# Optimization experiments

Hardware: AMD Instinct MI355X
Metric: run time of the kernel (lower is better)

The kernel has to match this reference:

```python
import jax, jax.numpy as jnp
import numpy as np

R_MAX = 5.0
NUM_BASIS = 8
CUTOFF_P = 6
N_LAYERS = 3
C = 64          # hidden_mul / channels of irreps_conv_out (64x0e+64x1o)
Z = 4           # element_number
AVG_DEG = 32.0  # num-neighbor normalization (E/N)
SQRT3 = 1.7320508075688772
SQRT2 = 1.4142135623730951


def _radial_embedding(r):
    # Bessel basis * polynomial cutoff (RadialEdgeEmbedding)
    rs = jnp.maximum(r, 1e-9)
    n = jnp.arange(1, NUM_BASIS + 1, dtype=r.dtype)  # (B,)
    bessel = jnp.sqrt(2.0 / R_MAX) * jnp.sin(n * jnp.pi * rs[:, None] / R_MAX) / rs[:, None]
    x = r / R_MAX
    p = float(CUTOFF_P)
    fc = (1.0
          - (p + 1.0) * (p + 2.0) / 2.0 * x ** CUTOFF_P
          + p * (p + 2.0) * x ** (CUTOFF_P + 1)
          - p * (p + 1.0) / 2.0 * x ** (CUTOFF_P + 2))
    fc = jnp.where(x < 1.0, fc, 0.0)
    return bessel * fc[:, None]  # (E, NUM_BASIS)


def setup_inputs() -> dict:
    key = jax.random.key(0)
    ks = jax.random.split(key, 20)
    N, E, B = 16000, 512000, 16
    atom_type = jax.random.randint(ks[0], (N,), 0, Z)
    # atoms in a 4A box so most edge lengths fall inside r_max=5
    atom_pos = jax.random.uniform(ks[1], (N, 3), dtype=jnp.float32) * 4.0
    edge_src = jax.random.randint(ks[2], (E,), 0, N)
    edge_dst = jax.random.randint(ks[3], (E,), 0, N)
    edge_cell_shift = jnp.zeros((E, 3), jnp.float32)
    cell = jnp.tile(jnp.eye(3, dtype=jnp.float32) * 10.0, (B, 1, 1)) \
        + 0.01 * jax.random.normal(ks[4], (B, 3, 3), jnp.float32)
    image_index = jax.random.randint(ks[5], (N,), 0, B)
    g = lambda k, s, fan: jax.random.normal(k, s, jnp.float32) / np.sqrt(fan)
    return {
        'atom_type': atom_type, 'atom_pos': atom_pos,
        'edge_src': edge_src, 'edge_dst': edge_dst,
        'edge_cell_shift': edge_cell_shift, 'cell': cell, 'image_index': image_index,
        'w_lin_in': g(ks[6], (Z, C), Z),
        'mlp_w1': g(ks[7], (N_LAYERS, NUM_BASIS, 64), NUM_BASIS),
        'mlp_b1': jnp.zeros((N_LAYERS, 64), jnp.float32),
        'mlp_w2': g(ks[8], (N_LAYERS, 64, 5 * C), 64),
        'w_self_s': g(ks[9], (N_LAYERS, C, C), C),
        'w_self_v': g(ks[10], (N_LAYERS, C, C), C),
        'w_gate': g(ks[11], (N_LAYERS, C, C), C),
        'w_lin1': g(ks[12], (C, 16), C),
        'w_lin2': g(ks[13], (16, 1), 16),
    }


def reference(atom_type, atom_pos, edge_src, edge_dst, edge_cell_shift, cell,
              image_index, w_lin_in, mlp_w1, mlp_b1, mlp_w2,
              w_self_s, w_self_v, w_gate, w_lin1, w_lin2):
    N = atom_pos.shape[0]
    # edge vectors with periodic cell shift
    edge_vec = atom_pos[edge_dst] - atom_pos[edge_src]
    edge_vec = edge_vec + jnp.einsum('ni,nij->nj', edge_cell_shift,
                                     cell.reshape(-1, 3, 3)[image_index[edge_src]])
    r = jnp.linalg.norm(edge_vec, axis=1)                      # (E,)
    unit = edge_vec / jnp.maximum(r, 1e-9)[:, None]
    # spherical harmonics lmax=1, component normalization: y0=1 (implicit), y1=sqrt(3)*unit
    y1 = SQRT3 * unit                                           # (E, 3)
    emb = _radial_embedding(r)                                  # (E, NUM_BASIS)

    # one-hot embedding + input linear (one-hot is all 0e -> scalar channels only)
    onehot = jax.nn.one_hot(atom_type, Z, dtype=atom_pos.dtype)
    s = onehot @ w_lin_in                                       # (N, C) l=0 features
    v = jnp.zeros((N, C, 3), atom_pos.dtype)                    # (N, C, 3) l=1 features

    inv_sqrt_deg = 1.0 / np.sqrt(AVG_DEG)
    for L in range(N_LAYERS):
        # radial MLP -> per-edge per-channel tensor-product path weights
        w = jax.nn.silu(emb @ mlp_w1[L] + mlp_b1[L]) @ mlp_w2[L]  # (E, 5C)
        w1, w2, w3, w4, w5 = jnp.split(w, 5, axis=1)              # (E, C) each
        s_src = s[edge_src]                                       # (E, C)
        v_src = v[edge_src]                                       # (E, C, 3)
        vdoty = jnp.einsum('ecx,ex->ec', v_src, y1)
        # CG tensor-product paths (l<=1):
        m_s = w1 * s_src + w2 * vdoty / SQRT3                     # 0x0->0, 1x1->0
        m_v = (w3[:, :, None] * s_src[:, :, None] * y1[:, None, :]      # 0x1->1
               + w4[:, :, None] * v_src                                  # 1x0->1
               + w5[:, :, None] * jnp.cross(v_src, y1[:, None, :]) / SQRT2)  # 1x1->1
        agg_s = jax.ops.segment_sum(m_s, edge_dst, num_segments=N) * inv_sqrt_deg
        agg_v = jax.ops.segment_sum(m_v, edge_dst, num_segments=N) * inv_sqrt_deg
        # gated self-interaction + resnet
        gate = jax.nn.sigmoid(agg_s @ w_gate[L])                  # (N, C)
        s = s + jax.nn.silu(agg_s @ w_self_s[L])
        v = v + jnp.einsum('ncx,cd->ndx', agg_v, w_self_v[L]) * gate[:, :, None]

    # o3.Linear to 16x0e then 1x0e (only scalar channels map to 0e outputs)
    atomic_energy = (s @ w_lin1) @ w_lin2                         # (N, 1)
    atomic_energy = atomic_energy * 1.0                           # atomic_scale
    return atomic_energy
```

## Files before the change

kernel.cpp:

```cpp
#include <hip/hip_runtime.h>
#include <hip/hip_fp16.h>
#include <math.h>

#define NUM_BASIS 8
#define SQRT3 1.7320508075688772f
#define SQRT2 1.4142135623730951f
#define INV_SQRT_DEG 0.17677669529663687f
#define PI_F 3.14159265358979323846f

typedef _Float16 half8 __attribute__((ext_vector_type(8)));
typedef float float4v __attribute__((ext_vector_type(4)));

__device__ __forceinline__ float sigmoidf_(float x) { return 1.0f / (1.0f + __expf(-x)); }
__device__ __forceinline__ float siluf_(float x) { return x * sigmoidf_(x); }

__device__ __forceinline__ void unp2(unsigned u, float& a, float& b) {
    __half2 h = *reinterpret_cast<__half2*>(&u);
    float2 f = __half22float2(h);
    a = f.x; b = f.y;
}
__device__ __forceinline__ unsigned pk2(float a, float b) {
    __half2 h = __floats2half2_rn(a, b);
    return *reinterpret_cast<unsigned*>(&h);
}

__global__ __launch_bounds__(256) void count_deg(
    const int* __restrict__ dst, int* __restrict__ deg, int E)
{
    int e = blockIdx.x * blockDim.x + threadIdx.x;
    if (e < E) atomicAdd(&deg[dst[e]], 1);
}

__global__ __launch_bounds__(1024) void scan_deg(
    const int* __restrict__ deg, int* __restrict__ cursor, int N)
{
    __shared__ int wsum[16];
    __shared__ int carry_s, tot_s;
    int tid = threadIdx.x;
    int wid = tid >> 6, lane = tid & 63;
    if (tid == 0) carry_s = 0;
    __syncthreads();
    for (int base = 0; base < N; base += 16384) {
        int i0 = base + tid * 16;
        int v[16];
        int sum = 0;
        #pragma unroll
        for (int k = 0; k < 16; k++) {
            int i = i0 + k;
            v[k] = (i < N) ? deg[i] : 0;
            sum += v[k];
        }
        int incl = sum;
        #pragma unroll
        for (int off = 1; off < 64; off <<= 1) {
            int t = __shfl_up(incl, off);
            if (lane >= off) incl += t;
        }
        if (lane == 63) wsum[wid] = incl;
        __syncthreads();
        if (wid == 0 && lane < 16) {
            int wv = wsum[lane];
            int wincl = wv;
            #pragma unroll
            for (int off = 1; off < 16; off <<= 1) {
                int t = __shfl_up(wincl, off);
                if (lane >= off) wincl += t;
            }
            wsum[lane] = wincl - wv;
            if (lane == 15) tot_s = wincl;
        }
        __syncthreads();
        int carry = carry_s;
        int run = carry + wsum[wid] + incl - sum;
        #pragma unroll
        for (int k = 0; k < 16; k++) {
            int i = i0 + k;
            if (i < N) cursor[i] = run;
            run += v[k];
        }
        __syncthreads();
        if (tid == 0) carry_s = carry + tot_s;
        __syncthreads();
    }
}

__global__ __launch_bounds__(256) void edge_pre_scatter(
    const float* __restrict__ pos, const int* __restrict__ src,
    const int* __restrict__ dst, const float* __restrict__ cs,
    const float* __restrict__ cell, const int* __restrict__ img,
    int* __restrict__ cursor, float* __restrict__ emb,
    float4* __restrict__ y14, int2* __restrict__ sdp, int E)
{
    int e = blockIdx.x * blockDim.x + threadIdx.x;
    if (e >= E) return;
    int si = src[e], di = dst[e];
    int slot = atomicAdd(&cursor[di], 1);
    sdp[slot] = make_int2(si, di);
    float vx = pos[di*3+0] - pos[si*3+0];
    float vy = pos[di*3+1] - pos[si*3+1];
    float vz = pos[di*3+2] - pos[si*3+2];
    float c0 = cs[(size_t)e*3+0], c1 = cs[(size_t)e*3+1], c2 = cs[(size_t)e*3+2];
    const float* M = cell + (size_t)img[si] * 9;
    vx += c0*M[0] + c1*M[3] + c2*M[6];
    vy += c0*M[1] + c1*M[4] + c2*M[7];
    vz += c0*M[2] + c1*M[5] + c2*M[8];
    float r  = sqrtf(vx*vx + vy*vy + vz*vz);
    float rs = fmaxf(r, 1e-9f);
    float inv = 1.0f / rs;
    y14[slot] = make_float4(SQRT3*vx*inv, SQRT3*vy*inv, SQRT3*vz*inv, 0.0f);
    float x = r * (1.0f / 5.0f);
    float x2 = x*x, x6 = x2*x2*x2;
    float fc = 1.0f - 28.0f*x6 + 48.0f*x6*x - 21.0f*x6*x2;
    if (x >= 1.0f) fc = 0.0f;
    float pre = sqrtf(2.0f / 5.0f) * inv * fc;
    float t = PI_F * rs * (1.0f / 5.0f);
    #pragma unroll
    for (int n = 1; n <= NUM_BASIS; n++)
        emb[(size_t)slot*NUM_BASIS + (n-1)] = pre * __sinf((float)n * t);
}

__global__ __launch_bounds__(256) void prep_weights(
    const float* __restrict__ W2, _Float16* __restrict__ w2f,
    const float* __restrict__ Wg, const float* __restrict__ Ws,
    const float* __restrict__ Wv, _Float16* __restrict__ wgtf,
    const float* __restrict__ Wl1, const float* __restrict__ Wl2,
    float* __restrict__ wl12)
{
    int idx = blockIdx.x * blockDim.x + threadIdx.x;
    if (idx < 64) {
        float a = 0.f;
        #pragma unroll
        for (int j = 0; j < 16; j++) a = fmaf(Wl1[idx*16 + j], Wl2[j], a);
        wl12[idx] = a;
    }
    if (idx < 3 * 20480) {
        int L  = idx / 20480;
        int r  = idx % 20480;
        int cg = r / 5120;
        int r2 = r % 5120;
        int p  = r2 / 1024;
        int r3 = r2 % 1024;
        int kh = r3 / 512;
        int r4 = r3 % 512;
        int lane = r4 / 8;
        int j  = r4 % 8;
        int k = kh*32 + (lane >> 4)*8 + j;
        int n = p*64 + cg*16 + (lane & 15);
        w2f[idx] = (_Float16)W2[(size_t)L*20480 + k*320 + n];
    } else if (idx < 3*20480 + 3*3*4096) {
        int idx2 = idx - 3*20480;
        int L   = idx2 / 12288;
        int rem = idx2 % 12288;
        int mat = rem / 4096;
        int r2  = rem % 4096;
        int cg  = r2 / 1024;
        int r3  = r2 % 1024;
        int kh  = r3 / 512;
        int r4  = r3 % 512;
        int lane = r4 / 8;
        int j   = r4 % 8;
        int k = kh*32 + (lane >> 4)*8 + j;
        int n = cg*16 + (lane & 15);
        const float* src = (mat == 0) ? Wg : (mat == 1) ? Ws : Wv;
        wgtf[idx2] = (_Float16)src[(size_t)L*4096 + k*64 + n];
    }
}

__device__ __forceinline__ void mlp1_afrag(
    const float* __restrict__ emb, const float* __restrict__ W1,
    const float* __restrict__ B1, int eA, int q, half8 afrag[2])
{
    float4 ea = *(const float4*)(emb + (size_t)eA*8);
    float4 eb2 = *(const float4*)(emb + (size_t)eA*8 + 4);
    float em[8] = {ea.x, ea.y, ea.z, ea.w, eb2.x, eb2.y, eb2.z, eb2.w};
    #pragma unroll
    for (int kh = 0; kh < 2; kh++) {
        int kb = kh*32 + q*8;
        float hv[8];
        float4 b0 = *(const float4*)(B1 + kb);
        float4 b1 = *(const float4*)(B1 + kb + 4);
        hv[0]=b0.x; hv[1]=b0.y; hv[2]=b0.z; hv[3]=b0.w;
        hv[4]=b1.x; hv[5]=b1.y; hv[6]=b1.z; hv[7]=b1.w;
        #pragma unroll
        for (int jj = 0; jj < 8; jj++) {
            float4 wa = *(const float4*)(W1 + jj*64 + kb);
            float4 wb = *(const float4*)(W1 + jj*64 + kb + 4);
            hv[0] = fmaf(em[jj], wa.x, hv[0]);
            hv[1] = fmaf(em[jj], wa.y, hv[1]);
            hv[2] = fmaf(em[jj], wa.z, hv[2]);
            hv[3] = fmaf(em[jj], wa.w, hv[3]);
            hv[4] = fmaf(em[jj], wb.x, hv[4]);
            hv[5] = fmaf(em[jj], wb.y, hv[5]);
            hv[6] = fmaf(em[jj], wb.z, hv[6]);
            hv[7] = fmaf(em[jj], wb.w, hv[7]);
        }
        #pragma unroll
        for (int j = 0; j < 8; j++)
            afrag[kh][j] = (_Float16)siluf_(hv[j]);
    }
}

__global__ __launch_bounds__(256) void edge_msg_mfma_l0(
    const float* __restrict__ emb, const float4* __restrict__ y14,
    const int2* __restrict__ sdp,
    const int* __restrict__ type, const float* __restrict__ wlin,
    const float* __restrict__ W1, const float* __restrict__ B1,
    const _Float16* __restrict__ w2f,
    float* __restrict__ aggs, float* __restrict__ aggx,
    float* __restrict__ aggy, float* __restrict__ aggz, int E)
{
    int wave  = (blockIdx.x * blockDim.x + threadIdx.x) >> 6;
    int lane  = threadIdx.x & 63;
    int wbase = wave * 16;
    if (wbase >= E) return;
    int q   = lane >> 4;
    int col = lane & 15;

    int eb = wbase + q*4;
    int d[4], tt[4];
    float4 y1v[4];
    #pragma unroll
    for (int r = 0; r < 4; r++) {
        int2 sv = sdp[eb + r];
        tt[r] = type[sv.x];
        d[r]  = sv.y;
        y1v[r] = y14[eb + r];
    }

    half8 afrag[2];
    mlp1_afrag(emb, W1, B1, wbase + col, q, afrag);

    int dnq = __shfl_down(d[0], 16);
    int nd3 = (q == 3) ? -1 : dnq;
    int df = d[0], dl = d[3];
    bool U = (df == dl);
    int dlp = __shfl_up(dl, 16);
    bool link = (q > 0) && (dlp == df);

    #pragma unroll
    for (int cg = 0; cg < 4; cg++) {
        float4v a1 = {0,0,0,0}, a3 = {0,0,0,0};
        const _Float16* wbp = w2f + ((size_t)cg*5*2*64*8) + (size_t)lane*8;
        {
            half8 b10 = *(const half8*)(wbp + ((size_t)(0*2 + 0))*64*8);
            half8 b11 = *(const half8*)(wbp + ((size_t)(0*2 + 1))*64*8);
            half8 b30 = *(const half8*)(wbp + ((size_t)(2*2 + 0))*64*8);
            half8 b31 = *(const half8*)(wbp + ((size_t)(2*2 + 1))*64*8);
            a1 = __builtin_amdgcn_mfma_f32_16x16x32_f16(afrag[0], b10, a1, 0, 0, 0);
            a1 = __builtin_amdgcn_mfma_f32_16x16x32_f16(afrag[1], b11, a1, 0, 0, 0);
            a3 = __builtin_amdgcn_mfma_f32_16x16x32_f16(afrag[0], b30, a3, 0, 0, 0);
            a3 = __builtin_amdgcn_mfma_f32_16x16x32_f16(afrag[1], b31, a3, 0, 0, 0);
        }
        int c = cg*16 + col;

        float ms[4], mx[4], my[4], mz[4];
        #pragma unroll
        for (int r = 0; r < 4; r++) {
            float s = wlin[tt[r]*64 + c];
            float w3s = a3[r] * s;
            ms[r] = a1[r] * s;
            mx[r] = w3s * y1v[r].x;
            my[r] = w3s * y1v[r].y;
            mz[r] = w3s * y1v[r].z;
        }
        #pragma unroll
        for (int r = 1; r < 4; r++) {
            if (d[r] == d[r-1]) {
                ms[r] += ms[r-1]; mx[r] += mx[r-1];
                my[r] += my[r-1]; mz[r] += mz[r-1];
            }
        }
        float Cs = 0.f, Cx = 0.f, Cy = 0.f, Cz = 0.f;
        #pragma unroll
        for (int it = 0; it < 3; it++) {
            float es = ms[3] + (U ? Cs : 0.f);
            float ex = mx[3] + (U ? Cx : 0.f);
            float ey = my[3] + (U ? Cy : 0.f);
            float ez = mz[3] + (U ? Cz : 0.f);
            float ts = __shfl_up(es, 16);
            float tx = __shfl_up(ex, 16);
            float ty = __shfl_up(ey, 16);
            float tz = __shfl_up(ez, 16);
            Cs = link ? ts : 0.f; Cx = link ? tx : 0.f;
            Cy = link ? ty : 0.f; Cz = link ? tz : 0.f;
        }
        bool hr = true;
        #pragma unroll
        for (int r = 0; r < 4; r++) {
            if (r > 0) hr = hr && (d[r] == d[r-1]);
            float fs = ms[r] + (hr ? Cs : 0.f);
            float fx = mx[r] + (hr ? Cx : 0.f);
            float fy = my[r] + (hr ? Cy : 0.f);
            float fz = mz[r] + (hr ? Cz : 0.f);
            int nd = (r < 3) ? d[r+1] : nd3;
            if (nd != d[r]) {
                size_t ai = (size_t)d[r]*64 + c;
                atomicAdd(aggs + ai, fs);
                atomicAdd(aggx + ai, fx);
                atomicAdd(aggy + ai, fy);
                atomicAdd(aggz + ai, fz);
            }
        }
    }
}

__global__ __launch_bounds__(256) void edge_msg_mfma(
    const float* __restrict__ emb, const float4* __restrict__ y14,
    const int2* __restrict__ sdp,
    const uint2* __restrict__ nf,
    const float* __restrict__ W1, const float* __restrict__ B1,
    const _Float16* __restrict__ w2f,
    float* __restrict__ aggs, float* __restrict__ aggx,
    float* __restrict__ aggy, float* __restrict__ aggz, int E)
{
    int wave  = (blockIdx.x * blockDim.x + threadIdx.x) >> 6;
    int lane  = threadIdx.x & 63;
    int wbase = wave * 16;
    if (wbase >= E) return;
    int q   = lane >> 4;
    int col = lane & 15;

    int eb = wbase + q*4;
    int d[4], si[4];
    float4 y1v[4];
    #pragma unroll
    for (int r = 0; r < 4; r++) {
        int2 sv = sdp[eb + r];
        si[r] = sv.x;
        d[r]  = sv.y;
        y1v[r] = y14[eb + r];
    }

    uint2 pf[4][4];
    #pragma unroll
    for (int r = 0; r < 4; r++) {
        size_t nb = (size_t)si[r] * 64 + col;
        pf[r][0] = nf[nb];
        pf[r][1] = nf[nb + 16];
        pf[r][2] = nf[nb + 32];
        pf[r][3] = nf[nb + 48];
    }

    half8 afrag[2];
    mlp1_afrag(emb, W1, B1, wbase + col, q, afrag);

    int dnq = __shfl_down(d[0], 16);
    int nd3 = (q == 3) ? -1 : dnq;
    int df = d[0], dl = d[3];
    bool U = (df == dl);
    int dlp = __shfl_up(dl, 16);
    bool link = (q > 0) && (dlp == df);

    #pragma unroll
    for (int cg = 0; cg < 4; cg++) {
        float4v acc[5];
        #pragma unroll
        for (int p = 0; p < 5; p++) acc[p] = (float4v){0.f, 0.f, 0.f, 0.f};
        const _Float16* wbp = w2f + ((size_t)cg*5*2*64*8) + (size_t)lane*8;
        #pragma unroll
        for (int p = 0; p < 5; p++) {
            half8 bf0 = *(const half8*)(wbp + ((size_t)(p*2 + 0))*64*8);
            half8 bf1 = *(const half8*)(wbp + ((size_t)(p*2 + 1))*64*8);
            acc[p] = __builtin_amdgcn_mfma_f32_16x16x32_f16(afrag[0], bf0, acc[p], 0, 0, 0);
            acc[p] = __builtin_amdgcn_mfma_f32_16x16x32_f16(afrag[1], bf1, acc[p], 0, 0, 0);
        }
        int c = cg*16 + col;

        float ms[4], mx[4], my[4], mz[4];
        #pragma unroll
        for (int r = 0; r < 4; r++) {
            float fsx, fvx, fvy, fvz;
            unp2(pf[r][cg].x, fsx, fvx);
            unp2(pf[r][cg].y, fvy, fvz);
            float yx = y1v[r].x, yy = y1v[r].y, yz = y1v[r].z;
            float w1 = acc[0][r], w2 = acc[1][r], w3 = acc[2][r];
            float w4 = acc[3][r], w5 = acc[4][r];
            float vdoty = fvx*yx + fvy*yy + fvz*yz;
            ms[r] = w1*fsx + w2*vdoty*(1.0f/SQRT3);
            float cx = fvy*yz - fvz*yy;
            float cy = fvz*yx - fvx*yz;
            float cz = fvx*yy - fvy*yx;
            mx[r] = w3*fsx*yx + w4*fvx + w5*cx*(1.0f/SQRT2);
            my[r] = w3*fsx*yy + w4*fvy + w5*cy*(1.0f/SQRT2);
            mz[r] = w3*fsx*yz + w4*fvz + w5*cz*(1.0f/SQRT2);
        }
        #pragma unroll
        for (int r = 1; r < 4; r++) {
            if (d[r] == d[r-1]) {
                ms[r] += ms[r-1]; mx[r] += mx[r-1];
                my[r] += my[r-1]; mz[r] += mz[r-1];
            }
        }
        float Cs = 0.f, Cx = 0.f, Cy = 0.f, Cz = 0.f;
        #pragma unroll
        for (int it = 0; it < 3; it++) {
            float es = ms[3] + (U ? Cs : 0.f);
            float ex = mx[3] + (U ? Cx : 0.f);
            float ey = my[3] + (U ? Cy : 0.f);
            float ez = mz[3] + (U ? Cz : 0.f);
            float ts = __shfl_up(es, 16);
            float tx = __shfl_up(ex, 16);
            float ty = __shfl_up(ey, 16);
            float tz = __shfl_up(ez, 16);
            Cs = link ? ts : 0.f; Cx = link ? tx : 0.f;
            Cy = link ? ty : 0.f; Cz = link ? tz : 0.f;
        }
        bool hr = true;
        #pragma unroll
        for (int r = 0; r < 4; r++) {
            if (r > 0) hr = hr && (d[r] == d[r-1]);
            float fs = ms[r] + (hr ? Cs : 0.f);
            float fx = mx[r] + (hr ? Cx : 0.f);
            float fy = my[r] + (hr ? Cy : 0.f);
            float fz = mz[r] + (hr ? Cz : 0.f);
            int nd = (r < 3) ? d[r+1] : nd3;
            if (nd != d[r]) {
                size_t ai = (size_t)d[r]*64 + c;
                atomicAdd(aggs + ai, fs);
                atomicAdd(aggx + ai, fx);
                atomicAdd(aggy + ai, fy);
                atomicAdd(aggz + ai, fz);
            }
        }
    }
}

__global__ __launch_bounds__(256) void node_update_mfma(
    uint2* __restrict__ nf,
    float* __restrict__ aggs, float* __restrict__ aggx,
    float* __restrict__ aggy, float* __restrict__ aggz,
    const _Float16* __restrict__ wgtf,
    const int* __restrict__ type, const float* __restrict__ wlin,
    const float* __restrict__ wl12,
    float* __restrict__ out, int first, int do_out, int N)
{
    int wave  = (blockIdx.x * blockDim.x + threadIdx.x) >> 6;
    int lane  = threadIdx.x & 63;
    int wbase = wave * 16;
    if (wbase >= N) return;
    int q = lane >> 4, col = lane & 15;

    int nodeA = wbase + col;
    if (nodeA >= N) nodeA = N - 1;
    size_t nb = (size_t)nodeA * 64 + q * 8;
    half8 af0[2], af1[2], af2[2], af3[2];
    #pragma unroll
    for (int kh = 0; kh < 2; kh++) {
        const float* p0 = aggs + nb + kh*32;
        const float* p1 = aggx + nb + kh*32;
        const float* p2 = aggy + nb + kh*32;
        const float* p3 = aggz + nb + kh*32;
        float4 a0 = *(const float4*)p0, b0 = *(const float4*)(p0+4);
        float4 a1 = *(const float4*)p1, b1 = *(const float4*)(p1+4);
        float4 a2 = *(const float4*)p2, b2 = *(const float4*)(p2+4);
        float4 a3 = *(const float4*)p3, b3 = *(const float4*)(p3+4);
        af0[kh][0]=(_Float16)(a0.x*INV_SQRT_DEG); af0[kh][1]=(_Float16)(a0.y*INV_SQRT_DEG);
        af0[kh][2]=(_Float16)(a0.z*INV_SQRT_DEG); af0[kh][3]=(_Float16)(a0.w*INV_SQRT_DEG);
        af0[kh][4]=(_Float16)(b0.x*INV_SQRT_DEG); af0[kh][5]=(_Float16)(b0.y*INV_SQRT_DEG);
        af0[kh][6]=(_Float16)(b0.z*INV_SQRT_DEG); af0[kh][7]=(_Float16)(b0.w*INV_SQRT_DEG);
        af1[kh][0]=(_Float16)(a1.x*INV_SQRT_DEG); af1[kh][1]=(_Float16)(a1.y*INV_SQRT_DEG);
        af1[kh][2]=(_Float16)(a1.z*INV_SQRT_DEG); af1[kh][3]=(_Float16)(a1.w*INV_SQRT_DEG);
        af1[kh][4]=(_Float16)(b1.x*INV_SQRT_DEG); af1[kh][5]=(_Float16)(b1.y*INV_SQRT_DEG);
        af1[kh][6]=(_Float16)(b1.z*INV_SQRT_DEG); af1[kh][7]=(_Float16)(b1.w*INV_SQRT_DEG);
        af2[kh][0]=(_Float16)(a2.x*INV_SQRT_DEG); af2[kh][1]=(_Float16)(a2.y*INV_SQRT_DEG);
        af2[kh][2]=(_Float16)(a2.z*INV_SQRT_DEG); af2[kh][3]=(_Float16)(a2.w*INV_SQRT_DEG);
        af2[kh][4]=(_Float16)(b2.x*INV_SQRT_DEG); af2[kh][5]=(_Float16)(b2.y*INV_SQRT_DEG);
        af2[kh][6]=(_Float16)(b2.z*INV_SQRT_DEG); af2[kh][7]=(_Float16)(b2.w*INV_SQRT_DEG);
        af3[kh][0]=(_Float16)(a3.x*INV_SQRT_DEG); af3[kh][1]=(_Float16)(a3.y*INV_SQRT_DEG);
        af3[kh][2]=(_Float16)(a3.z*INV_SQRT_DEG); af3[kh][3]=(_Float16)(a3.w*INV_SQRT_DEG);
        af3[kh][4]=(_Float16)(b3.x*INV_SQRT_DEG); af3[kh][5]=(_Float16)(b3.y*INV_SQRT_DEG);
        af3[kh][6]=(_Float16)(b3.z*INV_SQRT_DEG); af3[kh][7]=(_Float16)(b3.w*INV_SQRT_DEG);
    }

    int tt[4];
    #pragma unroll
    for (int r = 0; r < 4; r++) {
        int nd = wbase + q*4 + r;
        tt[r] = type[nd < N ? nd : 0];
    }

    float epart[4] = {0.f, 0.f, 0.f, 0.f};

    #pragma unroll
    for (int cg = 0; cg < 4; cg++) {
        const _Float16* bp = wgtf + (size_t)lane * 8;
        half8 bg0 = *(const half8*)(bp + ((size_t)((0*4 + cg)*2 + 0))*512);
        half8 bg1 = *(const half8*)(bp + ((size_t)((0*4 + cg)*2 + 1))*512);
        half8 bs0 = *(const half8*)(bp + ((size_t)((1*4 + cg)*2 + 0))*512);
        half8 bs1 = *(const half8*)(bp + ((size_t)((1*4 + cg)*2 + 1))*512);
        half8 bv0 = *(const half8*)(bp + ((size_t)((2*4 + cg)*2 + 0))*512);
        half8 bv1 = *(const half8*)(bp + ((size_t)((2*4 + cg)*2 + 1))*512);
        float4v ag = {0,0,0,0}, as = {0,0,0,0};
        float4v ox = {0,0,0,0}, oy = {0,0,0,0}, oz = {0,0,0,0};
        ag = __builtin_amdgcn_mfma_f32_16x16x32_f16(af0[0], bg0, ag, 0, 0, 0);
        ag = __builtin_amdgcn_mfma_f32_16x16x32_f16(af0[1], bg1, ag, 0, 0, 0);
        as = __builtin_amdgcn_mfma_f32_16x16x32_f16(af0[0], bs0, as, 0, 0, 0);
        as = __builtin_amdgcn_mfma_f32_16x16x32_f16(af0[1], bs1, as, 0, 0, 0);
        ox = __builtin_amdgcn_mfma_f32_16x16x32_f16(af1[0], bv0, ox, 0, 0, 0);
        ox = __builtin_amdgcn_mfma_f32_16x16x32_f16(af1[1], bv1, ox, 0, 0, 0);
        oy = __builtin_amdgcn_mfma_f32_16x16x32_f16(af2[0], bv0, oy, 0, 0, 0);
        oy = __builtin_amdgcn_mfma_f32_16x16x32_f16(af2[1], bv1, oy, 0, 0, 0);
        oz = __builtin_amdgcn_mfma_f32_16x16x32_f16(af3[0], bv0, oz, 0, 0, 0);
        oz = __builtin_amdgcn_mfma_f32_16x16x32_f16(af3[1], bv1, oz, 0, 0, 0);

        int c = cg*16 + col;
        float wlc = wl12[c];
        #pragma unroll
        for (int r = 0; r < 4; r++) {
            int nd = wbase + q*4 + r;
            bool wr = nd < N;
            size_t ni = (size_t)nd*64 + c;
            float sx, vx, vy, vz;
            if (first) {
                sx = wlin[tt[r]*64 + c];
                vx = 0.f; vy = 0.f; vz = 0.f;
            } else {
                uint2 cur = nf[wr ? ni : 0];
                unp2(cur.x, sx, vx);
                unp2(cur.y, vy, vz);
            }
            float gate = sigmoidf_(ag[r]);
            sx += siluf_(as[r]);
            vx += ox[r] * gate;
            vy += oy[r] * gate;
            vz += oz[r] * gate;
            if (wr) {
                uint2 nv;
                nv.x = pk2(sx, vx);
                nv.y = pk2(vy, vz);
                nf[ni] = nv;
                aggs[ni] = 0.f;
                aggx[ni] = 0.f;
                aggy[ni] = 0.f;
                aggz[ni] = 0.f;
                epart[r] = fmaf(sx, wlc, epart[r]);
            }
        }
    }
    if (do_out) {
        #pragma unroll
        for (int r = 0; r < 4; r++) {
            float e = epart[r];
            e += __shfl_xor(e, 1);
            e += __shfl_xor(e, 2);
            e += __shfl_xor(e, 4);
            e += __shfl_xor(e, 8);
            int nd = wbase + q*4 + r;
            if (col == 0 && nd < N) out[nd] = e;
        }
    }
}

extern "C" void kernel_launch(void* const* d_in, const int* in_sizes, int n_in,
                              void* d_out, int out_size, void* d_ws, size_t ws_size,
                              hipStream_t stream)
{
    const int*   atom_type = (const int*)  d_in[0];
    const float* pos       = (const float*)d_in[1];
    const int*   src       = (const int*)  d_in[2];
    const int*   dst       = (const int*)  d_in[3];
    const float* cs        = (const float*)d_in[4];
    const float* cell      = (const float*)d_in[5];
    const int*   img       = (const int*)  d_in[6];
    const float* wlin_in   = (const float*)d_in[7];
    const float* mw1       = (const float*)d_in[8];
    const float* mb1       = (const float*)d_in[9];
    const float* mw2       = (const float*)d_in[10];
    const float* wss       = (const float*)d_in[11];
    const float* wsv       = (const float*)d_in[12];
    const float* wg        = (const float*)d_in[13];
    const float* wl1       = (const float*)d_in[14];
    const float* wl2       = (const float*)d_in[15];
    int N = in_sizes[0];
    int E = in_sizes[2];

    char* w = (char*)d_ws;
    float*  emb  = (float*)w;  w += (size_t)E * 8 * sizeof(float);
    float4* y14  = (float4*)w; w += (size_t)E * sizeof(float4);
    int2*   sdp  = (int2*)w;   w += (size_t)E * sizeof(int2);
    uint2*  nf   = (uint2*)w;  w += (size_t)N * 64 * sizeof(uint2);
    float*  agg  = (float*)w;  w += (size_t)N * 64 * 4 * sizeof(float);
    _Float16* w2f  = (_Float16*)w; w += (size_t)3 * 20480 * sizeof(_Float16);
    _Float16* wgtf = (_Float16*)w; w += (size_t)3 * 3 * 4096 * sizeof(_Float16);
    float*  wl12 = (float*)w;  w += 64 * sizeof(float);
    int*    deg  = (int*)w;    w += (size_t)N * sizeof(int);
    int*    curs = (int*)w;    w += (size_t)N * sizeof(int);

    size_t NC = (size_t)N * 64;
    float* aggs = agg;
    float* aggx = agg + NC;
    float* aggy = agg + 2*NC;
    float* aggz = agg + 3*NC;

    hipMemsetAsync(deg, 0, (size_t)N * sizeof(int), stream);
    hipMemsetAsync(agg, 0, NC * 4 * sizeof(float), stream);
    count_deg<<<(E + 255) / 256, 256, 0, stream>>>(dst, deg, E);
    scan_deg<<<1, 1024, 0, stream>>>(deg, curs, N);
    int prep_n = 3*20480 + 3*3*4096;
    prep_weights<<<(prep_n + 255) / 256, 256, 0, stream>>>(
        mw2, w2f, wg, wss, wsv, wgtf, wl1, wl2, wl12);
    edge_pre_scatter<<<(E + 255) / 256, 256, 0, stream>>>(
        pos, src, dst, cs, cell, img, curs, emb, y14, sdp, E);

    int eblocks = (E + 63) / 64;
    int nblocks = (N + 63) / 64;

    edge_msg_mfma_l0<<<eblocks, 256, 0, stream>>>(
        emb, y14, sdp, atom_type, wlin_in,
        mw1, mb1, w2f, aggs, aggx, aggy, aggz, E);
    node_update_mfma<<<nblocks, 256, 0, stream>>>(
        nf, aggs, aggx, aggy, aggz, wgtf, atom_type, wlin_in, wl12,
        (float*)d_out, 1, 0, N);

    for (int L = 1; L < 3; L++) {
        edge_msg_mfma<<<eblocks, 256, 0, stream>>>(
            emb, y14, sdp, nf,
            mw1 + L * 8 * 64, mb1 + L * 64, w2f + (size_t)L * 20480,
            aggs, aggx, aggy, aggz, E);
        node_update_mfma<<<nblocks, 256, 0, stream>>>(
            nf, aggs, aggx, aggy, aggz,
            wgtf + (size_t)L * 12288, atom_type, wlin_in, wl12,
            (float*)d_out, 0, (L == 2) ? 1 : 0, N);
    }
}
```

Measured before the change: 525.7 us.

## Store edge embeddings and unit vectors in fp16 and drop cross-quad shuffle reduction

Edge radial embeddings and spherical-harmonic vectors are now stored as packed fp16 instead of fp32, halving their footprint and the bandwidth spent reading them in each of the three layers. The cross-quad carry chain built from wave shuffles is removed, so each quad of four edges now issues its own atomics when a destination run crosses a quad boundary. This cuts shuffle and select work but can raise atomic traffic on high-degree destinations, and fp16 storage lowers the precision of the geometric inputs.

Result: slower. 1.254 ms (+138.6%).

```diff
diff --git a/kernel.cpp b/kernel.cpp
--- a/kernel.cpp
+++ b/kernel.cpp
@@ -88,8 +88,8 @@
     const float* __restrict__ pos, const int* __restrict__ src,
     const int* __restrict__ dst, const float* __restrict__ cs,
     const float* __restrict__ cell, const int* __restrict__ img,
-    int* __restrict__ cursor, float* __restrict__ emb,
-    float4* __restrict__ y14, int2* __restrict__ sdp, int E)
+    int* __restrict__ cursor, _Float16* __restrict__ emb,
+    uint2* __restrict__ y14, int2* __restrict__ sdp, int E)
 {
     int e = blockIdx.x * blockDim.x + threadIdx.x;
     if (e >= E) return;
@@ -107,16 +107,21 @@
     float r  = sqrtf(vx*vx + vy*vy + vz*vz);
     float rs = fmaxf(r, 1e-9f);
     float inv = 1.0f / rs;
-    y14[slot] = make_float4(SQRT3*vx*inv, SQRT3*vy*inv, SQRT3*vz*inv, 0.0f);
+    uint2 yv;
+    yv.x = pk2(SQRT3*vx*inv, SQRT3*vy*inv);
+    yv.y = pk2(SQRT3*vz*inv, 0.f);
+    y14[slot] = yv;
     float x = r * (1.0f / 5.0f);
     float x2 = x*x, x6 = x2*x2*x2;
     float fc = 1.0f - 28.0f*x6 + 48.0f*x6*x - 21.0f*x6*x2;
     if (x >= 1.0f) fc = 0.0f;
     float pre = sqrtf(2.0f / 5.0f) * inv * fc;
     float t = PI_F * rs * (1.0f / 5.0f);
+    half8 ev;
     #pragma unroll
     for (int n = 1; n <= NUM_BASIS; n++)
-        emb[(size_t)slot*NUM_BASIS + (n-1)] = pre * __sinf((float)n * t);
+        ev[n-1] = (_Float16)(pre * __sinf((float)n * t));
+    *(half8*)(emb + (size_t)slot*NUM_BASIS) = ev;
 }
 
 __global__ __launch_bounds__(256) void prep_weights(
@@ -167,12 +172,13 @@
 }
 
 __device__ __forceinline__ void mlp1_afrag(
-    const float* __restrict__ emb, const float* __restrict__ W1,
+    const _Float16* __restrict__ emb, const float* __restrict__ W1,
     const float* __restrict__ B1, int eA, int q, half8 afrag[2])
 {
-    float4 ea = *(const float4*)(emb + (size_t)eA*8);
-    float4 eb2 = *(const float4*)(emb + (size_t)eA*8 + 4);
-    float em[8] = {ea.x, ea.y, ea.z, ea.w, eb2.x, eb2.y, eb2.z, eb2.w};
+    half8 ev = *(const half8*)(emb + (size_t)eA*8);
+    float em[8];
+    #pragma unroll
+    for (int j = 0; j < 8; j++) em[j] = (float)ev[j];
     #pragma unroll
     for (int kh = 0; kh < 2; kh++) {
         int kb = kh*32 + q*8;
@@ -201,7 +207,7 @@
 }
 
 __global__ __launch_bounds__(256) void edge_msg_mfma_l0(
-    const float* __restrict__ emb, const float4* __restrict__ y14,
+    const _Float16* __restrict__ emb, const uint2* __restrict__ y14,
     const int2* __restrict__ sdp,
     const int* __restrict__ type, const float* __restrict__ wlin,
     const float* __restrict__ W1, const float* __restrict__ B1,
@@ -218,24 +224,20 @@
 
     int eb = wbase + q*4;
     int d[4], tt[4];
-    float4 y1v[4];
+    float y1x[4], y1y[4], y1z[4];
     #pragma unroll
     for (int r = 0; r < 4; r++) {
         int2 sv = sdp[eb + r];
         tt[r] = type[sv.x];
         d[r]  = sv.y;
-        y1v[r] = y14[eb + r];
+        uint2 yv = y14[eb + r];
+        float dummy;
+        unp2(yv.x, y1x[r], y1y[r]);
+        unp2(yv.y, y1z[r], dummy);
     }
 
     half8 afrag[2];
     mlp1_afrag(emb, W1, B1, wbase + col, q, afrag);
-
-    int dnq = __shfl_down(d[0], 16);
-    int nd3 = (q == 3) ? -1 : dnq;
-    int df = d[0], dl = d[3];
-    bool U = (df == dl);
-    int dlp = __shfl_up(dl, 16);
-    bool link = (q > 0) && (dlp == df);
 
     #pragma unroll
     for (int cg = 0; cg < 4; cg++) {
@@ -259,9 +261,9 @@
             float s = wlin[tt[r]*64 + c];
             float w3s = a3[r] * s;
             ms[r] = a1[r] * s;
-            mx[r] = w3s * y1v[r].x;
-            my[r] = w3s * y1v[r].y;
-            mz[r] = w3s * y1v[r].z;
+            mx[r] = w3s * y1x[r];
+            my[r] = w3s * y1y[r];
+            mz[r] = w3s * y1z[r];
         }
         #pragma unroll
         for (int r = 1; r < 4; r++) {
@@ -270,42 +272,22 @@
                 my[r] += my[r-1]; mz[r] += mz[r-1];
             }
         }
-        float Cs = 0.f, Cx = 0.f, Cy = 0.f, Cz = 0.f;
-        #pragma unroll
-        for (int it = 0; it < 3; it++) {
-            float es = ms[3] + (U ? Cs : 0.f);
-            float ex = mx[3] + (U ? Cx : 0.f);
-            float ey = my[3] + (U ? Cy : 0.f);
-            float ez = mz[3] + (U ? Cz : 0.f);
-            float ts = __shfl_up(es, 16);
-            float tx = __shfl_up(ex, 16);
-            float ty = __shfl_up(ey, 16);
-            float tz = __shfl_up(ez, 16);
-            Cs = link ? ts : 0.f; Cx = link ? tx : 0.f;
-            Cy = link ? ty : 0.f; Cz = link ? tz : 0.f;
-        }
-        bool hr = true;
         #pragma unroll
         for (int r = 0; r < 4; r++) {
-            if (r > 0) hr = hr && (d[r] == d[r-1]);
-            float fs = ms[r] + (hr ? Cs : 0.f);
-            float fx = mx[r] + (hr ? Cx : 0.f);
-            float fy = my[r] + (hr ? Cy : 0.f);
-            float fz = mz[r] + (hr ? Cz : 0.f);
-            int nd = (r < 3) ? d[r+1] : nd3;
-            if (nd != d[r]) {
+            int ndx = (r < 3) ? d[r+1] : -2;
+            if (ndx != d[r] && d[r] >= 0) {
                 size_t ai = (size_t)d[r]*64 + c;
-                atomicAdd(aggs + ai, fs);
-                atomicAdd(aggx + ai, fx);
-                atomicAdd(aggy + ai, fy);
-                atomicAdd(aggz + ai, fz);
+                atomicAdd(aggs + ai, ms[r]);
+                atomicAdd(aggx + ai, mx[r]);
+                atomicAdd(aggy + ai, my[r]);
+                atomicAdd(aggz + ai, mz[r]);
             }
         }
     }
 }
 
 __global__ __launch_bounds__(256) void edge_msg_mfma(
-    const float* __restrict__ emb, const float4* __restrict__ y14,
+    const _Float16* __restrict__ emb, const uint2* __restrict__ y14,
     const int2* __restrict__ sdp,
     const uint2* __restrict__ nf,
     const float* __restrict__ W1, const float* __restrict__ B1,
@@ -322,13 +304,16 @@
 
     int eb = wbase + q*4;
     int d[4], si[4];
-    float4 y1v[4];
+    float y1x[4], y1y[4], y1z[4];
     #pragma unroll
     for (int r = 0; r < 4; r++) {
         int2 sv = sdp[eb + r];
         si[r] = sv.x;
         d[r]  = sv.y;
-        y1v[r] = y14[eb + r];
+        uint2 yv = y14[eb + r];
+        float dummy;
+        unp2(yv.x, y1x[r], y1y[r]);
+        unp2(yv.y, y1z[r], dummy);
     }
 
     uint2 pf[4][4];
@@ -344,13 +329,6 @@
     half8 afrag[2];
     mlp1_afrag(emb, W1, B1, wbase + col, q, afrag);
 
-    int dnq = __shfl_down(d[0], 16);
-    int nd3 = (q == 3) ? -1 : dnq;
-    int df = d[0], dl = d[3];
-    bool U = (df == dl);
-    int dlp = __shfl_up(dl, 16);
-    bool link = (q > 0) && (dlp == df);
-
     #pragma unroll
     for (int cg = 0; cg < 4; cg++) {
         float4v acc[5];
@@ -372,7 +350,7 @@
             float fsx, fvx, fvy, fvz;
             unp2(pf[r][cg].x, fsx, fvx);
             unp2(pf[r][cg].y, fvy, fvz);
-            float yx = y1v[r].x, yy = y1v[r].y, yz = y1v[r].z;
+            float yx = y1x[r], yy = y1y[r], yz = y1z[r];
             float w1 = acc[0][r], w2 = acc[1][r], w3 = acc[2][r];
             float w4 = acc[3][r], w5 = acc[4][r];
             float vdoty = fvx*yx + fvy*yy + fvz*yz;
@@ -391,35 +369,15 @@
                 my[r] += my[r-1]; mz[r] += mz[r-1];
             }
         }
-        float Cs = 0.f, Cx = 0.f, Cy = 0.f, Cz = 0.f;
-        #pragma unroll
-        for (int it = 0; it < 3; it++) {
-            float es = ms[3] + (U ? Cs : 0.f);
-            float ex = mx[3] + (U ? Cx : 0.f);
-            float ey = my[3] + (U ? Cy : 0.f);
-            float ez = mz[3] + (U ? Cz : 0.f);
-            float ts = __shfl_up(es, 16);
-            float tx = __shfl_up(ex, 16);
-            float ty = __shfl_up(ey, 16);
-            float tz = __shfl_up(ez, 16);
-            Cs = link ? ts : 0.f; Cx = link ? tx : 0.f;
-            Cy = link ? ty : 0.f; Cz = link ? tz : 0.f;
-        }
-        bool hr = true;
         #pragma unroll
         for (int r = 0; r < 4; r++) {
-            if (r > 0) hr = hr && (d[r] == d[r-1]);
-            float fs = ms[r] + (hr ? Cs : 0.f);
-            float fx = mx[r] + (hr ? Cx : 0.f);
-            float fy = my[r] + (hr ? Cy : 0.f);
-            float fz = mz[r] + (hr ? Cz : 0.f);
-            int nd = (r < 3) ? d[r+1] : nd3;
-            if (nd != d[r]) {
+            int ndx = (r < 3) ? d[r+1] : -2;
+            if (ndx != d[r] && d[r] >= 0) {
                 size_t ai = (size_t)d[r]*64 + c;
-                atomicAdd(aggs + ai, fs);
-                atomicAdd(aggx + ai, fx);
-                atomicAdd(aggy + ai, fy);
-                atomicAdd(aggz + ai, fz);
+                atomicAdd(aggs + ai, ms[r]);
+                atomicAdd(aggx + ai, mx[r]);
+                atomicAdd(aggy + ai, my[r]);
+                atomicAdd(aggz + ai, mz[r]);
             }
         }
     }
@@ -575,8 +533,8 @@
     int E = in_sizes[2];
 
     char* w = (char*)d_ws;
-    float*  emb  = (float*)w;  w += (size_t)E * 8 * sizeof(float);
-    float4* y14  = (float4*)w; w += (size_t)E * sizeof(float4);
+    _Float16* emb = (_Float16*)w; w += (size_t)E * 8 * sizeof(_Float16);
+    uint2*  y14  = (uint2*)w;  w += (size_t)E * sizeof(uint2);
     int2*   sdp  = (int2*)w;   w += (size_t)E * sizeof(int2);
     uint2*  nf   = (uint2*)w;  w += (size_t)N * 64 * sizeof(uint2);
     float*  agg  = (float*)w;  w += (size_t)N * 64 * 4 * sizeof(float);
```
